# Optimization experiments

Hardware: AMD Instinct MI355X
Metric: run time of the kernel (lower is better)

The kernel has to match this reference:

```python
import jax, jax.numpy as jnp
import numpy as np

F4_E2M1_MAX = 6.0
F8E4M3_MAX = 448.0
E4M3_EPS = 0.015625  # torch.finfo(float8_e4m3fn).tiny = 2**-6
BLOCK = 16
KE2M1 = jnp.array([0.0, 0.5, 1.0, 1.5, 2.0, 3.0, 4.0, 6.0], dtype=jnp.float32)


def round_to_e4m3(x):
    # emulate cast to float8_e4m3fn and back (round-to-nearest-even)
    return x.astype(jnp.float8_e4m3fn).astype(jnp.float32)


def fp4_121_positive(x):
    step1 = jnp.round(2.0 * x) / 2.0   # subnormal-ish region [0,2): step 0.5
    step2 = jnp.round(x)               # [2,4): step 1
    step3 = 2.0 * jnp.round(x / 2.0)   # [4,6]: step 2
    return jnp.where(x < 2.0, step1, jnp.where(x < 4.0, step2, step3))


def cast_to_fp4(x):
    return jnp.sign(x) * fp4_121_positive(jnp.abs(x))


def unpack_fp4_from_uint8(a, m, n):
    # a: int-typed tensor holding byte values in [0,256); two fp4 codes per byte
    high = (a.reshape(-1) >> 4) & 0xF
    low = a.reshape(-1) & 0xF
    combined = jnp.stack((low, high), axis=1).reshape(m, n)  # interleave low,high
    signs = (combined & 8) != 0
    abs_idx = combined & 7
    return KE2M1[abs_idx] * jnp.where(signs, -1.0, 1.0)


def dequant_nvfp4_packed(data_lp, out_scales, per_tensor_scale):
    m, half_n = data_lp.shape
    n = half_n * 2
    data_hp = unpack_fp4_from_uint8(data_lp, m, n)           # [m, n] float32
    scale_fp = out_scales / per_tensor_scale                  # [m, n/16]
    data_hp = data_hp.reshape(m, -1, BLOCK) * scale_fp.reshape(m, -1, 1)
    return data_hp.reshape(m, n)


def qdq_nvfp4(x):
    m, n = x.shape
    tensor_amax = jnp.max(jnp.abs(x))
    pts = jnp.clip(tensor_amax / F8E4M3_MAX, E4M3_EPS, F8E4M3_MAX)  # per-tensor scale
    xb = x.reshape(m, -1, BLOCK)
    block_scale = jnp.max(jnp.abs(xb), axis=-1) / F4_E2M1_MAX       # [m, n/16]
    scaled_bs = round_to_e4m3(jnp.clip(block_scale / pts, E4M3_EPS, F8E4M3_MAX))
    total_scale = pts * scaled_bs                                   # [m, n/16]
    data_scaled = jnp.clip(xb / total_scale[..., None], -F4_E2M1_MAX, F4_E2M1_MAX)
    data_lp = cast_to_fp4(data_scaled)                              # unpacked fp4 values
    # dequant: out_scales / (1/pts) == scaled_bs * pts == total_scale
    return (data_lp * total_scale[..., None]).reshape(m, n)


def setup_inputs() -> dict:
    key = jax.random.key(0)
    k1, k2, k3 = jax.random.split(key, 3)
    M, K, N = 16384, 2048, 2048  # tokens, in_features, out_features
    x = jax.random.normal(k1, (M, K), dtype=jnp.float32)
    weight_packed = jax.random.randint(k2, (N, K // 2), 0, 256, dtype=jnp.int32)
    # fp8-representable positive block scales
    weight_scale = round_to_e4m3(jax.random.uniform(k3, (N, K // 16), dtype=jnp.float32,
                                                    minval=0.05, maxval=1.0))
    weight_global_scale = jnp.ones((1,), dtype=jnp.float32)
    return {"x": x, "weight_packed": weight_packed,
            "weight_scale": weight_scale, "weight_global_scale": weight_global_scale}


def reference(x, weight_packed, weight_scale, weight_global_scale):
    hp_weight = dequant_nvfp4_packed(weight_packed, weight_scale, weight_global_scale)
    x_dq = qdq_nvfp4(x)
    return x_dq @ hp_weight.T
```

## Files before the change

kernel.cpp:

```cpp
#include <hip/hip_runtime.h>

typedef unsigned short u16;
typedef unsigned int u32;
typedef __attribute__((ext_vector_type(8))) short short8;
typedef __attribute__((ext_vector_type(4))) float floatx4;

static constexpr int M = 16384, N = 2048, K = 2048;


__device__ inline u16 f32_to_bf16(float x) {
    u32 u = __float_as_uint(x);
    u += 0x7FFFu + ((u >> 16) & 1u);
    return (u16)(u >> 16);
}

__device__ inline float e4m3_rne(float x) {
    u32 u = __float_as_uint(x);
    u += 0x7FFFFu + ((u >> 20) & 1u);
    u &= 0xFFF00000u;
    return __uint_as_float(u);
}

__device__ inline float fp4_dec(u32 c) {
    u32 e = (c >> 1) & 3u;
    float m = (float)(c & 1u);
    float v = e ? (2.0f + m) * (float)(1u << e) * 0.25f : 0.5f * m;
    return (c & 8u) ? -v : v;
}

__device__ inline float fp4_round_mag(float a) {
    if (a < 2.0f) return rintf(2.0f * a) * 0.5f;
    if (a < 4.0f) return rintf(a);
    return 2.0f * rintf(a * 0.5f);
}

__device__ inline float pts_from_amax(float amax) {
    return fminf(fmaxf(amax / 448.0f, 0.015625f), 448.0f);
}


__global__ void amax_part(const float4* __restrict__ x, float* __restrict__ part, int n4,
                          const int* __restrict__ wp, const float* __restrict__ wsc,
                          const float* __restrict__ wgs, u16* __restrict__ wq) {
    int idx = blockIdx.x * blockDim.x + threadIdx.x;
    int stride = gridDim.x * blockDim.x;
    float m = 0.0f;
    for (int i = idx; i < n4; i += stride) {
        float4 v = x[i];
        m = fmaxf(m, fmaxf(fmaxf(fabsf(v.x), fabsf(v.y)), fmaxf(fabsf(v.z), fabsf(v.w))));
    }

    float ginv = wgs[0];
#pragma unroll
    for (int g = 0; g < 4; g++) {
        int i = idx + g * 524288;
        int n = i >> 10;
        int kb = i & 1023;
        u32 byte = (u32)wp[i] & 0xFFu;
        float scale = wsc[(size_t)n * (K / 16) + (kb >> 3)] / ginv;
        float lo = fp4_dec(byte & 0xFu) * scale;
        float hi = fp4_dec((byte >> 4) & 0xFu) * scale;
        ((u32*)wq)[i] = (u32)f32_to_bf16(lo) | ((u32)f32_to_bf16(hi) << 16);
    }

#pragma unroll
    for (int off = 32; off > 0; off >>= 1)
        m = fmaxf(m, __shfl_down(m, off));
    __shared__ float sm[4];
    if ((threadIdx.x & 63) == 0) sm[threadIdx.x >> 6] = m;
    __syncthreads();
    if (threadIdx.x == 0)
        part[blockIdx.x] = fmaxf(fmaxf(sm[0], sm[1]), fmaxf(sm[2], sm[3]));
}


__global__ void amax_fin(const float* __restrict__ part, u32* __restrict__ out) {
    int t = threadIdx.x;
    float m = fmaxf(part[t], part[t + 1024]);
#pragma unroll
    for (int off = 32; off > 0; off >>= 1)
        m = fmaxf(m, __shfl_down(m, off));
    __shared__ float sm[16];
    if ((t & 63) == 0) sm[t >> 6] = m;
    __syncthreads();
    if (t < 16) {
        m = sm[t];
#pragma unroll
        for (int off = 8; off > 0; off >>= 1)
            m = fmaxf(m, __shfl_down(m, off));
        if (t == 0) *out = __float_as_uint(m);
    }
}


static constexpr int QB = (M * K / 4) / 256;

__global__ void prep(const float4* __restrict__ x, uint2* __restrict__ aq,
                     const u32* __restrict__ amax_bits) {
    int idx = blockIdx.x * blockDim.x + threadIdx.x;
    float4 v = x[idx];

    float bm = fmaxf(fmaxf(fabsf(v.x), fabsf(v.y)), fmaxf(fabsf(v.z), fabsf(v.w)));
    bm = fmaxf(bm, __shfl_xor(bm, 1));
    bm = fmaxf(bm, __shfl_xor(bm, 2));

    float pts = pts_from_amax(__uint_as_float(*amax_bits));
    float bs = bm / 6.0f;
    float sbs = e4m3_rne(fminf(fmaxf(bs / pts, 0.015625f), 448.0f));
    float ts = pts * sbs;

    float vf[4] = {v.x, v.y, v.z, v.w};
    u16 o[4];
#pragma unroll
    for (int i = 0; i < 4; i++) {
        float s = vf[i] / ts;
        s = fminf(fmaxf(s, -6.0f), 6.0f);
        float lp = copysignf(fp4_round_mag(fabsf(s)), s);
        o[i] = f32_to_bf16(lp * sbs);
    }
    aq[idx] = *(const uint2*)o;
}


#define GLDS(g, l)                                                              \
    __builtin_amdgcn_global_load_lds(                                           \
        (const __attribute__((address_space(1))) unsigned int*)(g),             \
        (__attribute__((address_space(3))) unsigned int*)(l), 16, 0, 0)

__global__ __launch_bounds__(512, 2) void gemm_bt(
    const u16* __restrict__ A, const u16* __restrict__ B,
    float* __restrict__ C, const u32* __restrict__ amax_bits, int bm_base)
{
    __shared__ u16 sh[2][2][2][8192];

    const int tid = threadIdx.x;
    const int w = tid >> 6, lane = tid & 63;

    const int id = blockIdx.x;
    const int xcd = id & 7;
    const int local = id >> 3;
    const int bm = bm_base + xcd * 4 + (local >> 3);
    const int bn = local & 7;

    const int wm = w >> 2, wn = w & 3;
    const int r16 = lane & 15, q = lane >> 4;

    floatx4 acc[8][4] = {};

    const int swz = (r16 & 7) << 4;
    const int aoff0 = r16 * 64 + (((q * 16) ^ swz) >> 1);
    const int aoff1 = r16 * 64 + (((64 + q * 16) ^ swz) >> 1);

    const int srow8 = lane >> 3;
    const int scol = ((lane & 7) ^ srow8) * 8;
    const u16* gA[2], * gB[2];
    gA[0] = A + (size_t)(bm * 256 + (w * 2 + 0) * 8 + srow8) * K + scol;
    gA[1] = A + (size_t)(bm * 256 + (w * 2 + 1) * 8 + srow8) * K + scol;
    gB[0] = B + (size_t)(bn * 256 + (w * 2 + 0) * 8 + srow8) * K + scol;
    gB[1] = B + (size_t)(bn * 256 + (w * 2 + 1) * 8 + srow8) * K + scol;

#define STG(buf, mat, half, ktc) do {                                           \
        const u16* _s0 = ((mat) ? gB[0] : gA[0]) + (size_t)(half) * 128 * K + (ktc); \
        const u16* _s1 = ((mat) ? gB[1] : gA[1]) + (size_t)(half) * 128 * K + (ktc); \
        GLDS(_s0, &sh[buf][mat][half][w * 1024]);                               \
        GLDS(_s1, &sh[buf][mat][half][w * 1024 + 512]);                         \
    } while (0)

    short8 aF[4][2], bF[4][2];

#define RD_A(buf, Qa) do {                                                      \
        const u16* _ar = &sh[buf][0][wm][(Qa) * 4096];                          \
        _Pragma("unroll") for (int _i = 0; _i < 4; _i++) {                      \
            aF[_i][0] = *(const short8*)(_ar + _i * 1024 + aoff0);              \
            aF[_i][1] = *(const short8*)(_ar + _i * 1024 + aoff1); }            \
    } while (0)

#define RD_B(buf, Qb) do {                                                      \
        const u16* _br = &sh[buf][1][wn >> 1][(wn & 1) * 4096 + (Qb) * 2048];   \
        _Pragma("unroll") for (int _j = 0; _j < 2; _j++) {                      \
            bF[(Qb) * 2 + _j][0] = *(const short8*)(_br + _j * 1024 + aoff0);   \
            bF[(Qb) * 2 + _j][1] = *(const short8*)(_br + _j * 1024 + aoff1); } \
    } while (0)

#define MMAQ(Qa, Qb)                                                            \
        _Pragma("unroll") for (int _i = 0; _i < 4; _i++)                        \
        _Pragma("unroll") for (int _j = 0; _j < 2; _j++)                        \
        _Pragma("unroll") for (int _k = 0; _k < 2; _k++)                        \
            acc[(Qa) * 4 + _i][(Qb) * 2 + _j] =                                 \
                __builtin_amdgcn_mfma_f32_16x16x32_bf16(                        \
                    aF[_i][_k], bF[(Qb) * 2 + _j][_k],                          \
                    acc[(Qa) * 4 + _i][(Qb) * 2 + _j], 0, 0, 0)

#define BAR do { __builtin_amdgcn_sched_barrier(0);                             \
                 __builtin_amdgcn_s_barrier();                                  \
                 __builtin_amdgcn_sched_barrier(0); } while (0)
#define PRIO1 __builtin_amdgcn_s_setprio(1)
#define PRIO0 do { __builtin_amdgcn_s_setprio(0);                               \
                   __builtin_amdgcn_sched_barrier(0); } while (0)
#define ENDPH do { __builtin_amdgcn_s_barrier();                                \
                   __builtin_amdgcn_sched_barrier(0); } while (0)
#define CHK4 do { asm volatile("s_waitcnt vmcnt(4)" ::: "memory");              \
                  __builtin_amdgcn_sched_barrier(0); } while (0)

    STG(0, 0, 0, 0); STG(0, 0, 1, 0);
    STG(0, 1, 0, 0); STG(0, 1, 1, 0);
    STG(1, 1, 0, 64); STG(1, 1, 1, 64);
    CHK4;
    __builtin_amdgcn_s_barrier();

#pragma unroll 1
    for (int it = 0; it < K / 128; ++it) {
        const int ktY  = (2 * it + 1) * 64;
        const int kx2  = 2 * it + 2, ky2 = 2 * it + 3;
        const int ktX2 = (kx2 <= 31 ? kx2 : 31) * 64;
        const int ktY2 = (ky2 <= 31 ? ky2 : 31) * 64;

        RD_A(0, 0); RD_B(0, 0); STG(1, 0, 0, ktY);
        BAR; PRIO1; MMAQ(0, 0); PRIO0; ENDPH;
        RD_B(0, 1); STG(1, 0, 1, ktY);
        BAR; PRIO1; MMAQ(0, 1); PRIO0; ENDPH;
        RD_A(0, 1); STG(0, 1, 0, ktX2); STG(0, 1, 1, ktX2);
        BAR; PRIO1; MMAQ(1, 1); MMAQ(1, 0); PRIO0; CHK4; ENDPH;
        RD_A(1, 0); RD_B(1, 0); STG(0, 0, 0, ktX2);
        BAR; PRIO1; MMAQ(0, 0); PRIO0; ENDPH;
        RD_B(1, 1); STG(0, 0, 1, ktX2);
        BAR; PRIO1; MMAQ(0, 1); PRIO0; ENDPH;
        RD_A(1, 1); STG(1, 1, 0, ktY2); STG(1, 1, 1, ktY2);
        BAR; PRIO1; MMAQ(1, 1); MMAQ(1, 0); PRIO0; CHK4; ENDPH;
    }

    asm volatile("s_waitcnt vmcnt(0)" ::: "memory");

    float pts = pts_from_amax(__uint_as_float(*amax_bits));

    float* Cb = C + (size_t)(bm * 256 + wm * 128 + q * 4) * N
                  + bn * 256 + wn * 64 + r16;
#pragma unroll
    for (int i = 0; i < 8; i++)
#pragma unroll
        for (int j = 0; j < 4; j++)
#pragma unroll
            for (int t = 0; t < 4; t++)
                Cb[(size_t)(i * 16 + t) * N + j * 16] = pts * acc[i][j][t];
}


extern "C" void kernel_launch(void* const* d_in, const int* in_sizes, int n_in,
                              void* d_out, int out_size, void* d_ws, size_t ws_size,
                              hipStream_t stream) {
    const float* x   = (const float*)d_in[0];
    const int*   wp  = (const int*)d_in[1];
    const float* wsc = (const float*)d_in[2];
    const float* wgs = (const float*)d_in[3];
    float* out = (float*)d_out;

    u32*   amax_ws = (u32*)d_ws;
    float* part    = (float*)((char*)d_ws + 64);
    u16*   aq      = (u16*)((char*)d_ws + 16384);
    u16*   wq      = aq + (size_t)M * K;

    amax_part<<<2048, 256, 0, stream>>>((const float4*)x, part, M * K / 4,
                                        wp, wsc, wgs, wq);
    amax_fin<<<1, 1024, 0, stream>>>(part, amax_ws);
    prep<<<QB, 256, 0, stream>>>((const float4*)x, (uint2*)aq, amax_ws);
    gemm_bt<<<256, 512, 0, stream>>>(aq, wq, out, amax_ws, 0);
    gemm_bt<<<256, 512, 0, stream>>>(aq, wq, out, amax_ws, 32);
}
```

Baseline: 385.2 us.

## Fuse amax finalize into partial pass, merge GEMM launches, stage C stores via LDS

```diff
diff --git a/kernel.cpp b/kernel.cpp
--- a/kernel.cpp
+++ b/kernel.cpp
@@ -39,15 +39,18 @@
 }
 
 
-__global__ void amax_part(const float4* __restrict__ x, float* __restrict__ part, int n4,
-                          const int* __restrict__ wp, const float* __restrict__ wsc,
-                          const float* __restrict__ wgs, u16* __restrict__ wq) {
+__global__ __launch_bounds__(256) void amax_part(
+    const float4* __restrict__ x, float* __restrict__ part,
+    const int* __restrict__ wp, const float* __restrict__ wsc,
+    const float* __restrict__ wgs, u16* __restrict__ wq,
+    u32* __restrict__ cnt, u32* __restrict__ amax_bits) {
     int idx = blockIdx.x * blockDim.x + threadIdx.x;
-    int stride = gridDim.x * blockDim.x;
     float m = 0.0f;
-    for (int i = idx; i < n4; i += stride) {
-        float4 v = x[i];
-        m = fmaxf(m, fmaxf(fmaxf(fabsf(v.x), fabsf(v.y)), fmaxf(fabsf(v.z), fabsf(v.w))));
+#pragma unroll 4
+    for (int it = 0; it < 16; ++it) {
+        float4 v = x[idx + it * 524288];
+        m = fmaxf(m, fmaxf(fmaxf(fabsf(v.x), fabsf(v.y)),
+                           fmaxf(fabsf(v.z), fabsf(v.w))));
     }
 
     float ginv = wgs[0];
@@ -67,58 +70,66 @@
     for (int off = 32; off > 0; off >>= 1)
         m = fmaxf(m, __shfl_down(m, off));
     __shared__ float sm[4];
+    __shared__ bool last;
     if ((threadIdx.x & 63) == 0) sm[threadIdx.x >> 6] = m;
     __syncthreads();
-    if (threadIdx.x == 0)
+    if (threadIdx.x == 0) {
         part[blockIdx.x] = fmaxf(fmaxf(sm[0], sm[1]), fmaxf(sm[2], sm[3]));
-}
-
-
-__global__ void amax_fin(const float* __restrict__ part, u32* __restrict__ out) {
-    int t = threadIdx.x;
-    float m = fmaxf(part[t], part[t + 1024]);
-#pragma unroll
-    for (int off = 32; off > 0; off >>= 1)
-        m = fmaxf(m, __shfl_down(m, off));
-    __shared__ float sm[16];
-    if ((t & 63) == 0) sm[t >> 6] = m;
+        __threadfence();
+        u32 d = __hip_atomic_fetch_add(cnt, 1u, __ATOMIC_ACQ_REL,
+                                       __HIP_MEMORY_SCOPE_AGENT);
+        last = (d == 2047u);
+    }
     __syncthreads();
-    if (t < 16) {
-        m = sm[t];
-#pragma unroll
-        for (int off = 8; off > 0; off >>= 1)
-            m = fmaxf(m, __shfl_down(m, off));
-        if (t == 0) *out = __float_as_uint(m);
-    }
-}
-
-
-static constexpr int QB = (M * K / 4) / 256;
-
-__global__ void prep(const float4* __restrict__ x, uint2* __restrict__ aq,
-                     const u32* __restrict__ amax_bits) {
-    int idx = blockIdx.x * blockDim.x + threadIdx.x;
-    float4 v = x[idx];
-
-    float bm = fmaxf(fmaxf(fabsf(v.x), fabsf(v.y)), fmaxf(fabsf(v.z), fabsf(v.w)));
-    bm = fmaxf(bm, __shfl_xor(bm, 1));
-    bm = fmaxf(bm, __shfl_xor(bm, 2));
-
+    if (last) {
+        __threadfence();
+        int t = threadIdx.x;
+        float r = 0.0f;
+#pragma unroll
+        for (int i = 0; i < 8; i++) r = fmaxf(r, part[t + i * 256]);
+#pragma unroll
+        for (int off = 32; off > 0; off >>= 1)
+            r = fmaxf(r, __shfl_down(r, off));
+        if ((t & 63) == 0) sm[t >> 6] = r;
+        __syncthreads();
+        if (t == 0)
+            *amax_bits = __float_as_uint(
+                fmaxf(fmaxf(sm[0], sm[1]), fmaxf(sm[2], sm[3])));
+    }
+}
+
+
+__global__ __launch_bounds__(256) void prep(
+    const float4* __restrict__ x, uint2* __restrict__ aq,
+    const u32* __restrict__ amax_bits) {
+    int idx0 = blockIdx.x * blockDim.x + threadIdx.x;
     float pts = pts_from_amax(__uint_as_float(*amax_bits));
-    float bs = bm / 6.0f;
-    float sbs = e4m3_rne(fminf(fmaxf(bs / pts, 0.015625f), 448.0f));
-    float ts = pts * sbs;
-
-    float vf[4] = {v.x, v.y, v.z, v.w};
-    u16 o[4];
-#pragma unroll
-    for (int i = 0; i < 4; i++) {
-        float s = vf[i] / ts;
-        s = fminf(fmaxf(s, -6.0f), 6.0f);
-        float lp = copysignf(fp4_round_mag(fabsf(s)), s);
-        o[i] = f32_to_bf16(lp * sbs);
-    }
-    aq[idx] = *(const uint2*)o;
+
+#pragma unroll 4
+    for (int it = 0; it < 16; ++it) {
+        int idx = idx0 + it * 524288;
+        float4 v = x[idx];
+
+        float bm = fmaxf(fmaxf(fabsf(v.x), fabsf(v.y)),
+                         fmaxf(fabsf(v.z), fabsf(v.w)));
+        bm = fmaxf(bm, __shfl_xor(bm, 1));
+        bm = fmaxf(bm, __shfl_xor(bm, 2));
+
+        float bs = bm / 6.0f;
+        float sbs = e4m3_rne(fminf(fmaxf(bs / pts, 0.015625f), 448.0f));
+        float ts = pts * sbs;
+
+        float vf[4] = {v.x, v.y, v.z, v.w};
+        u16 o[4];
+#pragma unroll
+        for (int i = 0; i < 4; i++) {
+            float s = vf[i] / ts;
+            s = fminf(fmaxf(s, -6.0f), 6.0f);
+            float lp = copysignf(fp4_round_mag(fabsf(s)), s);
+            o[i] = f32_to_bf16(lp * sbs);
+        }
+        aq[idx] = *(const uint2*)o;
+    }
 }
 
 
@@ -129,7 +140,7 @@
 
 __global__ __launch_bounds__(512, 2) void gemm_bt(
     const u16* __restrict__ A, const u16* __restrict__ B,
-    float* __restrict__ C, const u32* __restrict__ amax_bits, int bm_base)
+    float* __restrict__ C, const u32* __restrict__ amax_bits)
 {
     __shared__ u16 sh[2][2][2][8192];
 
@@ -139,7 +150,7 @@
     const int id = blockIdx.x;
     const int xcd = id & 7;
     const int local = id >> 3;
-    const int bm = bm_base + xcd * 4 + (local >> 3);
+    const int bm = xcd * 8 + (local >> 3);
     const int bn = local & 7;
 
     const int wm = w >> 2, wn = w & 3;
@@ -230,18 +241,32 @@
     }
 
     asm volatile("s_waitcnt vmcnt(0)" ::: "memory");
+    __builtin_amdgcn_s_barrier();
+    __builtin_amdgcn_sched_barrier(0);
 
     float pts = pts_from_amax(__uint_as_float(*amax_bits));
 
-    float* Cb = C + (size_t)(bm * 256 + wm * 128 + q * 4) * N
-                  + bn * 256 + wn * 64 + r16;
-#pragma unroll
-    for (int i = 0; i < 8; i++)
+    float* stage = (float*)&sh[0][0][0][0] + w * 1024;
+    const int erow = lane >> 4;
+    const int ecol = lane & 15;
+    float* Cb = C + (size_t)(bm * 256 + wm * 128) * N + bn * 256 + wn * 64;
+#pragma unroll
+    for (int i = 0; i < 8; i++) {
 #pragma unroll
         for (int j = 0; j < 4; j++)
 #pragma unroll
             for (int t = 0; t < 4; t++)
-                Cb[(size_t)(i * 16 + t) * N + j * 16] = pts * acc[i][j][t];
+                stage[(q * 4 + t) * 64 + j * 16 + r16] = pts * acc[i][j][t];
+        asm volatile("s_waitcnt lgkmcnt(0)" ::: "memory");
+        __builtin_amdgcn_sched_barrier(0);
+#pragma unroll
+        for (int k4 = 0; k4 < 4; k4++) {
+            float4 vv = *(const float4*)&stage[(k4 * 4 + erow) * 64 + ecol * 4];
+            *(float4*)&Cb[(size_t)(i * 16 + k4 * 4 + erow) * N + ecol * 4] = vv;
+        }
+        asm volatile("s_waitcnt lgkmcnt(0)" ::: "memory");
+        __builtin_amdgcn_sched_barrier(0);
+    }
 }
 
 
@@ -254,15 +279,15 @@
     const float* wgs = (const float*)d_in[3];
     float* out = (float*)d_out;
 
-    u32*   amax_ws = (u32*)d_ws;
-    float* part    = (float*)((char*)d_ws + 64);
-    u16*   aq      = (u16*)((char*)d_ws + 16384);
-    u16*   wq      = aq + (size_t)M * K;
-
-    amax_part<<<2048, 256, 0, stream>>>((const float4*)x, part, M * K / 4,
-                                        wp, wsc, wgs, wq);
-    amax_fin<<<1, 1024, 0, stream>>>(part, amax_ws);
-    prep<<<QB, 256, 0, stream>>>((const float4*)x, (uint2*)aq, amax_ws);
-    gemm_bt<<<256, 512, 0, stream>>>(aq, wq, out, amax_ws, 0);
-    gemm_bt<<<256, 512, 0, stream>>>(aq, wq, out, amax_ws, 32);
-}
+    u32*   cnt       = (u32*)d_ws;
+    u32*   amax_bits = (u32*)((char*)d_ws + 4);
+    float* part      = (float*)((char*)d_ws + 64);
+    u16*   aq        = (u16*)((char*)d_ws + 16384);
+    u16*   wq        = aq + (size_t)M * K;
+
+    hipMemsetAsync(d_ws, 0, 64, stream);
+    amax_part<<<2048, 256, 0, stream>>>((const float4*)x, part,
+                                        wp, wsc, wgs, wq, cnt, amax_bits);
+    prep<<<2048, 256, 0, stream>>>((const float4*)x, (uint2*)aq, amax_bits);
+    gemm_bt<<<512, 512, 0, stream>>>(aq, wq, out, amax_bits);
+}
```

After: 491.6 us. 27.6% more time.
